# Optimization experiments

Measured on AMD Instinct MI355X. Metric: run time of the kernel, lower is better.

## Reference

```python
import jax, jax.numpy as jnp
import numpy as np

B, S, DIM, H = 1, 4096, 1024, 16
HEAD_DIM = DIM // H
ROPE_THETA = 10000.0
LN_EPS = 1e-5


def _rope_cos_sin(seq_len, dim, theta):
    # frequencies over the FULL model dim (rope applied before head split, as in source)
    inv_freq = 1.0 / (theta ** (jnp.arange(0, dim, 2, dtype=jnp.float32) / dim))  # (dim/2,)
    ang = jnp.arange(seq_len, dtype=jnp.float32)[:, None] * inv_freq[None, :]     # (S, dim/2)
    cos = jnp.concatenate([jnp.cos(ang), jnp.cos(ang)], axis=-1)                  # (S, dim)
    sin = jnp.concatenate([jnp.sin(ang), jnp.sin(ang)], axis=-1)
    return cos, sin


def _rotate_half(x):
    d = x.shape[-1] // 2
    return jnp.concatenate([-x[..., d:], x[..., :d]], axis=-1)


def _apply_rope(x, cos, sin):
    # x: (B, S, dim); cos/sin: (S, dim)
    return x * cos[None] + _rotate_half(x) * sin[None]


def setup_inputs() -> dict:
    key = jax.random.key(0)
    ks = jax.random.split(key, 5)
    sc = 1.0 / np.sqrt(DIM)
    return {
        "x": jax.random.normal(ks[0], (B, S, DIM), dtype=jnp.float32),
        "Wqkv": jax.random.normal(ks[1], (DIM, 3 * DIM), dtype=jnp.float32) * sc,
        "bqkv": jax.random.normal(ks[2], (3 * DIM,), dtype=jnp.float32) * 0.01,
        "Wo": jax.random.normal(ks[3], (DIM, DIM), dtype=jnp.float32) * sc,
        "bo": jax.random.normal(ks[4], (DIM,), dtype=jnp.float32) * 0.01,
        "gamma": jnp.ones((DIM,), dtype=jnp.float32),
        "beta": jnp.zeros((DIM,), dtype=jnp.float32),
    }


def reference(x, Wqkv, bqkv, Wo, bo, gamma, beta):
    b, s, d = x.shape
    qkv = x @ Wqkv + bqkv                      # (B, S, 3*dim)
    q, k, v = jnp.split(qkv, 3, axis=-1)       # each (B, S, dim)
    cos, sin = _rope_cos_sin(s, d, ROPE_THETA)
    q = _apply_rope(q, cos, sin)
    k = _apply_rope(k, cos, sin)
    # split heads
    q = q.reshape(b, s, H, HEAD_DIM)
    k = k.reshape(b, s, H, HEAD_DIM)
    v = v.reshape(b, s, H, HEAD_DIM)
    scale = 1.0 / np.sqrt(HEAD_DIM)
    scores = jnp.einsum('bqhd,bkhd->bhqk', q, k) * scale  # (B, H, S, S)
    causal = jnp.triu(jnp.ones((s, s), dtype=bool), k=1)
    scores = jnp.where(causal[None, None], -jnp.inf, scores)
    attn = jax.nn.softmax(scores, axis=-1)
    out = jnp.einsum('bhqk,bkhd->bqhd', attn, v).reshape(b, s, d)
    out = out @ Wo + bo
    # LayerNorm (dropout is identity in eval mode)
    mu = jnp.mean(out, axis=-1, keepdims=True)
    var = jnp.mean(jnp.square(out - mu), axis=-1, keepdims=True)
    return (out - mu) * jax.lax.rsqrt(var + LN_EPS) * gamma + beta
```

## Files before the change

### kernel.cpp

```cpp
#include <hip/hip_runtime.h>
#include <cstdint>
#include <cstddef>

#define S_LEN 4096
#define DIM   1024
#define NH    16
#define HD    64
#define QKV_N 3072

typedef __attribute__((ext_vector_type(8))) short short8;
typedef __attribute__((ext_vector_type(4))) float f32x4;
typedef __attribute__((ext_vector_type(16))) float f32x16;
typedef __attribute__((ext_vector_type(4))) unsigned short ushort4v;
typedef __attribute__((ext_vector_type(2))) unsigned int uint2v;
typedef __attribute__((ext_vector_type(4))) unsigned int uint4v;

__device__ inline unsigned short f2bf(float x) {
    unsigned int u = __builtin_bit_cast(unsigned int, x);
    u += 0x7fffu + ((u >> 16) & 1u);
    return (unsigned short)(u >> 16);
}
__device__ inline float bf2f(unsigned short u) {
    return __builtin_bit_cast(float, (unsigned int)u << 16);
}
__device__ inline unsigned int pack2_bf16_rh(float lo, float hi) {
    unsigned int a = __builtin_bit_cast(unsigned int, lo) + 0x8000u;
    unsigned int b = __builtin_bit_cast(unsigned int, hi) + 0x8000u;
    return __builtin_amdgcn_perm(b, a, 0x07060302u);
}

__device__ inline void gl_lds16(const void* g, void* l) {
    __builtin_amdgcn_global_load_lds(
        (const __attribute__((address_space(1))) void*)g,
        (__attribute__((address_space(3))) void*)l, 16, 0, 0);
}

template <bool BF16OUT>
__global__ __launch_bounds__(256) void gemm_mfma_kernel(
    const unsigned short* __restrict__ A,
    const unsigned short* __restrict__ Bt,
    const float* __restrict__ bias,
    void* __restrict__ Cv,
    int M, int N, int K)
{
    __shared__ unsigned short As[128 * 32];
    __shared__ unsigned short Bs[128 * 32];

    const int t    = threadIdx.x;
    const int w    = t >> 6;
    const int lane = t & 63;
    const int ln   = lane & 15;
    const int quad = lane >> 4;
    const int bm   = blockIdx.y * 128;
    const int bn   = blockIdx.x * 128;
    const int wm   = (w & 1) * 64;
    const int wn   = (w >> 1) * 64;

    f32x4 acc[4][4];
#pragma unroll
    for (int i = 0; i < 4; ++i)
#pragma unroll
        for (int j = 0; j < 4; ++j) acc[i][j] = (f32x4){0.f, 0.f, 0.f, 0.f};

    const int lr = lane >> 2;
    const int lc = (lane & 3) * 8;
    const unsigned short* ga = A  + (size_t)(bm + w * 32 + lr) * K + lc;
    const unsigned short* gb = Bt + (size_t)(bn + w * 32 + lr) * K + lc;
    unsigned short* la = &As[(w * 32) * 32];
    unsigned short* lb = &Bs[(w * 32) * 32];

    for (int k0 = 0; k0 < K; k0 += 32) {
        gl_lds16(ga,            la);
        gl_lds16(ga + 16 * K,   la + 16 * 32);
        gl_lds16(gb,            lb);
        gl_lds16(gb + 16 * K,   lb + 16 * 32);
        ga += 32; gb += 32;
        __syncthreads();

        short8 af[4], bf[4];
#pragma unroll
        for (int i = 0; i < 4; ++i)
            af[i] = *(const short8*)&As[(wm + i * 16 + ln) * 32 + quad * 8];
#pragma unroll
        for (int j = 0; j < 4; ++j)
            bf[j] = *(const short8*)&Bs[(wn + j * 16 + ln) * 32 + quad * 8];
#pragma unroll
        for (int i = 0; i < 4; ++i)
#pragma unroll
            for (int j = 0; j < 4; ++j)
                acc[i][j] = __builtin_amdgcn_mfma_f32_16x16x32_bf16(af[i], bf[j], acc[i][j], 0, 0, 0);
        __syncthreads();
    }

#pragma unroll
    for (int j = 0; j < 4; ++j) {
        const int col = bn + wn + j * 16 + ln;
        const float bv = bias[col];
#pragma unroll
        for (int i = 0; i < 4; ++i) {
            const int row0 = bm + wm + i * 16 + quad * 4;
#pragma unroll
            for (int r = 0; r < 4; ++r) {
                const float v = acc[i][j][r] + bv;
                if (BF16OUT)
                    ((unsigned short*)Cv)[(size_t)(row0 + r) * N + col] = f2bf(v);
                else
                    ((float*)Cv)[(size_t)(row0 + r) * N + col] = v;
            }
        }
    }
}

__global__ __launch_bounds__(256) void prep1_kernel(
    const float* __restrict__ x, unsigned short* __restrict__ xb,
    const float* __restrict__ Wqkv, unsigned short* __restrict__ WqkvT,
    const float* __restrict__ Wo, unsigned short* __restrict__ WoT)
{
    __shared__ unsigned short L[64][72];
    const int b = blockIdx.x;
    const int t = threadIdx.x;

    if (b < 2048) {
        const size_t i = ((size_t)b * 256 + t) * 8;
        float4 a = *(const float4*)(x + i);
        float4 c = *(const float4*)(x + i + 4);
        short8 p = { (short)f2bf(a.x), (short)f2bf(a.y), (short)f2bf(a.z), (short)f2bf(a.w),
                     (short)f2bf(c.x), (short)f2bf(c.y), (short)f2bf(c.z), (short)f2bf(c.w) };
        *(short8*)(xb + i) = p;
        return;
    }
    const float* W;
    unsigned short* Wt;
    int N, n0, k0;
    if (b < 2816) {
        const int wb = b - 2048;
        W = Wqkv; Wt = WqkvT; N = QKV_N;
        n0 = (wb % 48) * 64; k0 = (wb / 48) * 64;
    } else {
        const int wb = b - 2816;
        W = Wo; Wt = WoT; N = DIM;
        n0 = (wb & 15) * 64; k0 = (wb >> 4) * 64;
    }
    const int kr = t >> 2, cb = (t & 3) * 16;
    const float* wp = W + (size_t)(k0 + kr) * N + n0 + cb;
#pragma unroll
    for (int u = 0; u < 16; u += 4) {
        float4 v = *(const float4*)(wp + u);
        ushort4v p = { f2bf(v.x), f2bf(v.y), f2bf(v.z), f2bf(v.w) };
        *(ushort4v*)&L[kr][cb + u] = p;
    }
    __syncthreads();
    const int nr = t >> 2, kb = (t & 3) * 16;
    short8 lo, hi;
#pragma unroll
    for (int u = 0; u < 8; ++u) lo[u] = (short)L[kb + u][nr];
#pragma unroll
    for (int u = 0; u < 8; ++u) hi[u] = (short)L[kb + 8 + u][nr];
    unsigned short* op = Wt + (size_t)(n0 + nr) * 1024 + k0 + kb;
    *(short8*)op       = lo;
    *(short8*)(op + 8) = hi;
}

__global__ __launch_bounds__(256) void prep2_kernel(
    const unsigned short* __restrict__ qkvb,
    unsigned short* __restrict__ Qb,
    unsigned short* __restrict__ Kb,
    unsigned short* __restrict__ Vt)
{
    __shared__ unsigned short L[64][72];
    const int b = blockIdx.x;
    const int t = threadIdx.x;

    if (b < 2048) {
        const int idx = b * 256 + t;
        const int j   = (idx & 127) * 4;
        const int s   = idx >> 7;
        const unsigned short* row = qkvb + (size_t)s * QKV_N;
        unsigned short* qo = Qb + (size_t)s * DIM;
        unsigned short* ko = Kb + (size_t)s * DIM;
        const float sf = (float)s;
        const float QSCALE = 0.18033688011112042f;
        const float C1 = -0.025952563241307517f;
        const float INV2PI = 0.15915494309189535f;

        float cs[4], sn[4];
#pragma unroll
        for (int e = 0; e < 4; ++e) {
            const float invf2pi = exp2f((float)(j + e) * C1) * INV2PI;
            float rev = sf * invf2pi;
            rev -= floorf(rev);
            sn[e] = __builtin_amdgcn_sinf(rev);
            cs[e] = __builtin_amdgcn_cosf(rev);
        }
        ushort4v q1 = *(const ushort4v*)(row + j);
        ushort4v q2 = *(const ushort4v*)(row + 512 + j);
        ushort4v k1 = *(const ushort4v*)(row + DIM + j);
        ushort4v k2 = *(const ushort4v*)(row + DIM + 512 + j);
        ushort4v qa, qb4, ka, kb4;
#pragma unroll
        for (int e = 0; e < 4; ++e) {
            const float x1 = bf2f(q1[e]), x2 = bf2f(q2[e]);
            const float y1 = bf2f(k1[e]), y2 = bf2f(k2[e]);
            qa[e]  = f2bf((x1 * cs[e] - x2 * sn[e]) * QSCALE);
            qb4[e] = f2bf((x2 * cs[e] + x1 * sn[e]) * QSCALE);
            ka[e]  = f2bf(y1 * cs[e] - y2 * sn[e]);
            kb4[e] = f2bf(y2 * cs[e] + y1 * sn[e]);
        }
        *(ushort4v*)(qo + j)       = qa;
        *(ushort4v*)(qo + 512 + j) = qb4;
        *(ushort4v*)(ko + j)       = ka;
        *(ushort4v*)(ko + 512 + j) = kb4;
        return;
    }

    const int vb = b - 2048;
    const int c0 = (vb & 15) * 64;
    const int bs = (vb >> 4) * 64;
    const int sl = t >> 2, cb = (t & 3) * 16;
    const unsigned short* vp = qkvb + (size_t)(bs + sl) * QKV_N + 2 * DIM + c0 + cb;
    *(short8*)&L[sl][cb]     = *(const short8*)vp;
    *(short8*)&L[sl][cb + 8] = *(const short8*)(vp + 8);
    __syncthreads();
    const int cl = t >> 2, sb = (t & 3) * 16;
    short8 lo, hi;
#pragma unroll
    for (int u = 0; u < 8; ++u) lo[u] = (short)L[sb + u][cl];
#pragma unroll
    for (int u = 0; u < 8; ++u) hi[u] = (short)L[sb + 8 + u][cl];
    unsigned short* op = Vt + (size_t)(c0 + cl) * S_LEN + bs + sb;
    *(short8*)op       = lo;
    *(short8*)(op + 8) = hi;
}

__global__ __launch_bounds__(256) void attn_mfma_kernel(
    const unsigned short* __restrict__ Qb,
    const unsigned short* __restrict__ Kb,
    const unsigned short* __restrict__ Vt,
    float* __restrict__ Op,
    float* __restrict__ lp)
{
    __shared__ unsigned short Ks[2][64 * 64];
    __shared__ unsigned short Vs[2][64 * 64];

    const int t    = threadIdx.x;
    const int w    = t >> 6;
    const int lane = t & 63;
    const int r31  = lane & 31;
    const int hi   = lane >> 5;
    const int p    = blockIdx.x;
    const int half = blockIdx.y;
    const int h    = blockIdx.z;

    const int srow  = t >> 2;
    const int sch   = (t & 3) * 2;
    const int ssw   = srow & 7;
    const int soff0 = srow * 64 + ((sch ^ ssw) << 3);
    const int soff1 = srow * 64 + (((sch + 1) ^ ssw) << 3);

    const int rA = r31 * 64;
    const int sw = r31 & 7;

#pragma unroll
    for (int phase = 0; phase < 2; ++phase) {
        const int qt  = phase == 0 ? (31 - p) : p;
        const int q0  = qt * 128;
        const int nkt = 2 * qt + 2;
        const int c0  = nkt >> 1;
        const int kt_begin = half == 0 ? 0 : c0;
        const int kt_end   = half == 0 ? c0 : nkt;

        short8 qf[4];
        {
            const unsigned short* qp = Qb + (size_t)(q0 + w * 32 + r31) * DIM + h * HD + hi * 8;
#pragma unroll
            for (int kk = 0; kk < 4; ++kk) qf[kk] = *(const short8*)(qp + kk * 16);
        }

        f32x16 o0 = {}, o1 = {};
        float lrow = 0.f;

        short8 kr0, kr1, vr0, vr1;
        {
            const int k0 = kt_begin * 64;
            const unsigned short* kp = Kb + (size_t)(k0 + srow) * DIM + h * HD + sch * 8;
            kr0 = *(const short8*)kp;  kr1 = *(const short8*)(kp + 8);
            const unsigned short* vp = Vt + (size_t)(h * HD + srow) * S_LEN + k0 + sch * 8;
            vr0 = *(const short8*)vp;  vr1 = *(const short8*)(vp + 8);
        }
        __syncthreads();

        for (int kt = kt_begin; kt < kt_end; ++kt) {
            const int buf = (kt - kt_begin) & 1;
            unsigned short* ks = &Ks[buf][0];
            unsigned short* vs = &Vs[buf][0];
            *(short8*)&ks[soff0] = kr0;
            *(short8*)&ks[soff1] = kr1;
            *(short8*)&vs[soff0] = vr0;
            *(short8*)&vs[soff1] = vr1;
            if (kt + 1 < kt_end) {
                const int k1 = (kt + 1) * 64;
                const unsigned short* kp = Kb + (size_t)(k1 + srow) * DIM + h * HD + sch * 8;
                kr0 = *(const short8*)kp;  kr1 = *(const short8*)(kp + 8);
                const unsigned short* vp = Vt + (size_t)(h * HD + srow) * S_LEN + k1 + sch * 8;
                vr0 = *(const short8*)vp;  vr1 = *(const short8*)(vp + 8);
            }
            __syncthreads();

            f32x16 s0 = {}, s1 = {};
#pragma unroll
            for (int kk = 0; kk < 4; ++kk) {
                const int co = (((kk * 2 + hi) ^ sw) << 3);
                short8 kf0 = *(const short8*)&ks[rA + co];
                short8 kf1 = *(const short8*)&ks[rA + 2048 + co];
                s0 = __builtin_amdgcn_mfma_f32_32x32x16_bf16(kf0, qf[kk], s0, 0, 0, 0);
                s1 = __builtin_amdgcn_mfma_f32_32x32x16_bf16(kf1, qf[kk], s1, 0, 0, 0);
            }

            if (kt >= nkt - 2) {
                const int qg = q0 + w * 32 + r31;
                const int kb = kt * 64 + 4 * hi;
#pragma unroll
                for (int g = 0; g < 4; ++g)
#pragma unroll
                    for (int a = 0; a < 4; ++a) {
                        const int keyl = kb + a + 8 * g;
                        if (keyl > qg)      s0[4 * g + a] = -1e30f;
                        if (keyl + 32 > qg) s1[4 * g + a] = -1e30f;
                    }
            }

            unsigned int pd0[8], pd1[8];
            float ps = 0.f;
#pragma unroll
            for (int g = 0; g < 4; ++g) {
                const float a0 = exp2f(s0[4 * g + 0]), a1 = exp2f(s0[4 * g + 1]);
                const float a2 = exp2f(s0[4 * g + 2]), a3 = exp2f(s0[4 * g + 3]);
                const float b0 = exp2f(s1[4 * g + 0]), b1 = exp2f(s1[4 * g + 1]);
                const float b2 = exp2f(s1[4 * g + 2]), b3 = exp2f(s1[4 * g + 3]);
                ps += ((a0 + a1) + (a2 + a3)) + ((b0 + b1) + (b2 + b3));
                pd0[2 * g]     = pack2_bf16_rh(a0, a1);
                pd0[2 * g + 1] = pack2_bf16_rh(a2, a3);
                pd1[2 * g]     = pack2_bf16_rh(b0, b1);
                pd1[2 * g + 1] = pack2_bf16_rh(b2, b3);
            }
            ps += __shfl_xor(ps, 32);
            lrow += ps;

#pragma unroll
            for (int w16 = 0; w16 < 4; ++w16) {
                const int lw = w16 & 1;
                unsigned int a0, b0, a1, b1;
                if (w16 < 2) { a0 = pd0[4 * lw];     b0 = pd0[4 * lw + 2];
                               a1 = pd0[4 * lw + 1]; b1 = pd0[4 * lw + 3]; }
                else         { a0 = pd1[4 * lw];     b0 = pd1[4 * lw + 2];
                               a1 = pd1[4 * lw + 1]; b1 = pd1[4 * lw + 3]; }
                asm("v_permlane32_swap_b32 %0, %1" : "+v"(a0), "+v"(b0));
                asm("v_permlane32_swap_b32 %0, %1" : "+v"(a1), "+v"(b1));
                const uint4v frw = { a0, a1, b0, b1 };
                const short8 pf = __builtin_bit_cast(short8, frw);
                const int co = (((w16 * 2 + hi) ^ sw) << 3);
                short8 vf0 = *(const short8*)&vs[rA + co];
                short8 vf1 = *(const short8*)&vs[rA + 2048 + co];
                o0 = __builtin_amdgcn_mfma_f32_32x32x16_bf16(vf0, pf, o0, 0, 0, 0);
                o1 = __builtin_amdgcn_mfma_f32_32x32x16_bf16(vf1, pf, o1, 0, 0, 0);
            }
        }

        {
            float* op = Op + ((size_t)half * S_LEN + q0 + w * 32 + r31) * DIM + h * HD + hi * 4;
#pragma unroll
            for (int g = 0; g < 4; ++g) {
                f32x4 v0 = { o0[4 * g + 0], o0[4 * g + 1], o0[4 * g + 2], o0[4 * g + 3] };
                f32x4 v1 = { o1[4 * g + 0], o1[4 * g + 1], o1[4 * g + 2], o1[4 * g + 3] };
                *(f32x4*)(op + g * 8)      = v0;
                *(f32x4*)(op + 32 + g * 8) = v1;
            }
            if (hi == 0)
                lp[((size_t)half * NH + h) * S_LEN + q0 + w * 32 + r31] = lrow;
        }
    }
}

__global__ __launch_bounds__(256) void combine_kernel(
    const float* __restrict__ Op, const float* __restrict__ lp,
    unsigned short* __restrict__ attnb)
{
    const int row = blockIdx.x;
    const int t   = threadIdx.x;
    const int d   = t * 4;
    const int h   = t >> 4;
    f32x4 a = *(const f32x4*)&Op[(size_t)row * DIM + d];
    f32x4 b = *(const f32x4*)&Op[((size_t)S_LEN + row) * DIM + d];
    const float l = lp[(size_t)h * S_LEN + row] + lp[((size_t)NH + h) * S_LEN + row];
    const float inv = 1.0f / l;
    ushort4v o;
#pragma unroll
    for (int e = 0; e < 4; ++e) o[e] = f2bf((a[e] + b[e]) * inv);
    *(ushort4v*)&attnb[(size_t)row * DIM + d] = o;
}

__global__ __launch_bounds__(256) void ln_kernel(
    const float* __restrict__ in, const float* __restrict__ gamma,
    const float* __restrict__ beta, float* __restrict__ out)
{
    const int row = blockIdx.x;
    const int t = threadIdx.x;
    const float4 v = *(const float4*)&in[(size_t)row * DIM + t * 4];
    float s  = v.x + v.y + v.z + v.w;
    float sq = v.x * v.x + v.y * v.y + v.z * v.z + v.w * v.w;
#pragma unroll
    for (int off = 1; off < 64; off <<= 1) {
        s  += __shfl_xor(s, off);
        sq += __shfl_xor(sq, off);
    }
    __shared__ float red[8];
    const int wv = t >> 6, ln = t & 63;
    if (ln == 0) { red[wv] = s; red[4 + wv] = sq; }
    __syncthreads();
    s  = red[0] + red[1] + red[2] + red[3];
    sq = red[4] + red[5] + red[6] + red[7];
    const float mu  = s * (1.0f / DIM);
    const float var = sq * (1.0f / DIM) - mu * mu;
    const float rs  = rsqrtf(var + 1e-5f);
    const float4 g = *(const float4*)&gamma[t * 4];
    const float4 b = *(const float4*)&beta[t * 4];
    float4 o = { (v.x - mu) * rs * g.x + b.x,
                 (v.y - mu) * rs * g.y + b.y,
                 (v.z - mu) * rs * g.z + b.z,
                 (v.w - mu) * rs * g.w + b.w };
    *(float4*)&out[(size_t)row * DIM + t * 4] = o;
}

extern "C" void kernel_launch(void* const* d_in, const int* in_sizes, int n_in,
                              void* d_out, int out_size, void* d_ws, size_t ws_size,
                              hipStream_t stream)
{
    const float* x     = (const float*)d_in[0];
    const float* Wqkv  = (const float*)d_in[1];
    const float* bqkv  = (const float*)d_in[2];
    const float* Wo    = (const float*)d_in[3];
    const float* bo    = (const float*)d_in[4];
    const float* gamma = (const float*)d_in[5];
    const float* beta  = (const float*)d_in[6];
    float* out = (float*)d_out;

    char* base = (char*)d_ws;
    unsigned short* qkvb  = (unsigned short*)base;
    unsigned short* attnb = (unsigned short*)base;
    float* Op   = (float*)(base + (size_t)8 * 1024 * 1024);
    float* proj = (float*)(base + (size_t)8 * 1024 * 1024);
    float* lp   = (float*)(base + (size_t)40 * 1024 * 1024);
    unsigned short* Qb    = (unsigned short*)(base + (size_t)48 * 1024 * 1024);
    unsigned short* Kb    = (unsigned short*)(base + (size_t)56 * 1024 * 1024);
    unsigned short* Vt    = (unsigned short*)(base + (size_t)64 * 1024 * 1024);
    unsigned short* xb    = (unsigned short*)(base + (size_t)72 * 1024 * 1024);
    unsigned short* WqkvT = (unsigned short*)(base + (size_t)80 * 1024 * 1024);
    unsigned short* WoT   = (unsigned short*)(base + (size_t)86 * 1024 * 1024);

    prep1_kernel<<<3072, 256, 0, stream>>>(x, xb, Wqkv, WqkvT, Wo, WoT);

    gemm_mfma_kernel<true><<<dim3(QKV_N / 128, S_LEN / 128), 256, 0, stream>>>(
        xb, WqkvT, bqkv, qkvb, S_LEN, QKV_N, DIM);

    prep2_kernel<<<3072, 256, 0, stream>>>(qkvb, Qb, Kb, Vt);

    attn_mfma_kernel<<<dim3(16, 2, NH), 256, 0, stream>>>(Qb, Kb, Vt, Op, lp);

    combine_kernel<<<S_LEN, 256, 0, stream>>>(Op, lp, attnb);

    gemm_mfma_kernel<false><<<dim3(DIM / 128, S_LEN / 128), 256, 0, stream>>>(
        attnb, WoT, bo, proj, S_LEN, DIM, DIM);

    ln_kernel<<<S_LEN, 256, 0, stream>>>(proj, gamma, beta, out);
}
```

Baseline: 248.6 us.

## Split attention KV range four ways and store partial outputs as bf16

Splits each query tile's key range into four chunks instead of two, doubling the attention grid to 16x4x16 blocks to fill more CUs. Partial outputs are written as bf16 rather than fp32 to limit the extra traffic, and the combine kernel sums the four partials and row-sums. This adds combine-pass reads and bf16 rounding of unnormalized partials. It also relies on the softmax using a shared fixed max across splits, since only row sums are combined.

```diff
diff --git a/kernel.cpp b/kernel.cpp
--- a/kernel.cpp
+++ b/kernel.cpp
@@ -7,6 +7,7 @@
 #define NH    16
 #define HD    64
 #define QKV_N 3072
+#define NSPLIT 4
 
 typedef __attribute__((ext_vector_type(8))) short short8;
 typedef __attribute__((ext_vector_type(4))) float f32x4;
@@ -236,7 +237,7 @@
     const unsigned short* __restrict__ Qb,
     const unsigned short* __restrict__ Kb,
     const unsigned short* __restrict__ Vt,
-    float* __restrict__ Op,
+    unsigned short* __restrict__ Opb,
     float* __restrict__ lp)
 {
     __shared__ unsigned short Ks[2][64 * 64];
@@ -248,7 +249,7 @@
     const int r31  = lane & 31;
     const int hi   = lane >> 5;
     const int p    = blockIdx.x;
-    const int half = blockIdx.y;
+    const int spl  = blockIdx.y;
     const int h    = blockIdx.z;
 
     const int srow  = t >> 2;
@@ -265,9 +266,8 @@
         const int qt  = phase == 0 ? (31 - p) : p;
         const int q0  = qt * 128;
         const int nkt = 2 * qt + 2;
-        const int c0  = nkt >> 1;
-        const int kt_begin = half == 0 ? 0 : c0;
-        const int kt_end   = half == 0 ? c0 : nkt;
+        const int kt_begin = (nkt * spl) / NSPLIT;
+        const int kt_end   = (nkt * (spl + 1)) / NSPLIT;
 
         short8 qf[4];
         {
@@ -367,35 +367,43 @@
         }
 
         {
-            float* op = Op + ((size_t)half * S_LEN + q0 + w * 32 + r31) * DIM + h * HD + hi * 4;
+            unsigned short* op = Opb + ((size_t)spl * S_LEN + q0 + w * 32 + r31) * DIM + h * HD + hi * 4;
 #pragma unroll
             for (int g = 0; g < 4; ++g) {
-                f32x4 v0 = { o0[4 * g + 0], o0[4 * g + 1], o0[4 * g + 2], o0[4 * g + 3] };
-                f32x4 v1 = { o1[4 * g + 0], o1[4 * g + 1], o1[4 * g + 2], o1[4 * g + 3] };
-                *(f32x4*)(op + g * 8)      = v0;
-                *(f32x4*)(op + 32 + g * 8) = v1;
+                ushort4v v0 = { f2bf(o0[4 * g + 0]), f2bf(o0[4 * g + 1]),
+                                f2bf(o0[4 * g + 2]), f2bf(o0[4 * g + 3]) };
+                ushort4v v1 = { f2bf(o1[4 * g + 0]), f2bf(o1[4 * g + 1]),
+                                f2bf(o1[4 * g + 2]), f2bf(o1[4 * g + 3]) };
+                *(ushort4v*)(op + g * 8)      = v0;
+                *(ushort4v*)(op + 32 + g * 8) = v1;
             }
             if (hi == 0)
-                lp[((size_t)half * NH + h) * S_LEN + q0 + w * 32 + r31] = lrow;
+                lp[((size_t)spl * NH + h) * S_LEN + q0 + w * 32 + r31] = lrow;
         }
     }
 }
 
 __global__ __launch_bounds__(256) void combine_kernel(
-    const float* __restrict__ Op, const float* __restrict__ lp,
+    const unsigned short* __restrict__ Opb, const float* __restrict__ lp,
     unsigned short* __restrict__ attnb)
 {
     const int row = blockIdx.x;
     const int t   = threadIdx.x;
     const int d   = t * 4;
     const int h   = t >> 4;
-    f32x4 a = *(const f32x4*)&Op[(size_t)row * DIM + d];
-    f32x4 b = *(const f32x4*)&Op[((size_t)S_LEN + row) * DIM + d];
-    const float l = lp[(size_t)h * S_LEN + row] + lp[((size_t)NH + h) * S_LEN + row];
+    float acc[4] = {0.f, 0.f, 0.f, 0.f};
+    float l = 0.f;
+#pragma unroll
+    for (int s = 0; s < NSPLIT; ++s) {
+        ushort4v a = *(const ushort4v*)&Opb[((size_t)s * S_LEN + row) * DIM + d];
+#pragma unroll
+        for (int e = 0; e < 4; ++e) acc[e] += bf2f(a[e]);
+        l += lp[((size_t)s * NH + h) * S_LEN + row];
+    }
     const float inv = 1.0f / l;
     ushort4v o;
 #pragma unroll
-    for (int e = 0; e < 4; ++e) o[e] = f2bf((a[e] + b[e]) * inv);
+    for (int e = 0; e < 4; ++e) o[e] = f2bf(acc[e] * inv);
     *(ushort4v*)&attnb[(size_t)row * DIM + d] = o;
 }
 
@@ -447,7 +455,7 @@
     char* base = (char*)d_ws;
     unsigned short* qkvb  = (unsigned short*)base;
     unsigned short* attnb = (unsigned short*)base;
-    float* Op   = (float*)(base + (size_t)8 * 1024 * 1024);
+    unsigned short* Opb   = (unsigned short*)(base + (size_t)8 * 1024 * 1024);
     float* proj = (float*)(base + (size_t)8 * 1024 * 1024);
     float* lp   = (float*)(base + (size_t)40 * 1024 * 1024);
     unsigned short* Qb    = (unsigned short*)(base + (size_t)48 * 1024 * 1024);
@@ -464,9 +472,9 @@
 
     prep2_kernel<<<3072, 256, 0, stream>>>(qkvb, Qb, Kb, Vt);
 
-    attn_mfma_kernel<<<dim3(16, 2, NH), 256, 0, stream>>>(Qb, Kb, Vt, Op, lp);
-
-    combine_kernel<<<S_LEN, 256, 0, stream>>>(Op, lp, attnb);
+    attn_mfma_kernel<<<dim3(16, NSPLIT, NH), 256, 0, stream>>>(Qb, Kb, Vt, Opb, lp);
+
+    combine_kernel<<<S_LEN, 256, 0, stream>>>(Opb, lp, attnb);
 
     gemm_mfma_kernel<false><<<dim3(DIM / 128, S_LEN / 128), 256, 0, stream>>>(
         attnb, WoT, bo, proj, S_LEN, DIM, DIM);
```

Result: slower. 256.5 us (+3.2%).
